# Optimization experiments

Measured on AMD Instinct MI355X. Metric: run time of the kernel, lower is better.

## Reference

```python
import jax, jax.numpy as jnp
import numpy as np
import math

DIM = 1024
N_HEADS = 16
HEAD_DIM = DIM // N_HEADS
FFN_HIDDEN = 4096
EPS = 1e-6


def setup_inputs() -> dict:
    key = jax.random.key(0)
    ks = jax.random.split(key, 10)
    s = 1.0 / math.sqrt(DIM)
    sh = 1.0 / math.sqrt(FFN_HIDDEN)
    return {
        "x": jax.random.normal(ks[0], (2, 2048, DIM), dtype=jnp.float32),
        # attention weights stored as [in, out] (y = x @ W)
        "wq": jax.random.normal(ks[1], (DIM, DIM), dtype=jnp.float32) * s,
        "wk": jax.random.normal(ks[2], (DIM, DIM), dtype=jnp.float32) * s,
        "wv": jax.random.normal(ks[3], (DIM, DIM), dtype=jnp.float32) * s,
        "wo": jax.random.normal(ks[4], (DIM, DIM), dtype=jnp.float32) * s,
        "w_gate": jax.random.normal(ks[5], (DIM, FFN_HIDDEN), dtype=jnp.float32) * s,
        "w_up": jax.random.normal(ks[6], (DIM, FFN_HIDDEN), dtype=jnp.float32) * s,
        "w_down": jax.random.normal(ks[7], (FFN_HIDDEN, DIM), dtype=jnp.float32) * sh,
        "attn_norm_w": jnp.ones((DIM,), dtype=jnp.float32),
        "ffn_norm_w": jnp.ones((DIM,), dtype=jnp.float32),
    }


def rmsnorm(x, w):
    xf = x.astype(jnp.float32)
    rms = jax.lax.rsqrt(jnp.mean(xf * xf, axis=-1, keepdims=True) + EPS)
    return (xf * rms).astype(x.dtype) * w


def attention(x, wq, wk, wv, wo):
    B, T, C = x.shape
    q = (x @ wq).reshape(B, T, N_HEADS, HEAD_DIM)
    k = (x @ wk).reshape(B, T, N_HEADS, HEAD_DIM)
    v = (x @ wv).reshape(B, T, N_HEADS, HEAD_DIM)
    scores = jnp.einsum("bqhd,bkhd->bhqk", q, k) / math.sqrt(HEAD_DIM)
    causal = jnp.tril(jnp.ones((T, T), dtype=bool))  # True = keep
    scores = jnp.where(causal, scores, -jnp.inf)
    attn = jax.nn.softmax(scores, axis=-1)
    out = jnp.einsum("bhqk,bkhd->bqhd", attn, v).reshape(B, T, C)
    return out @ wo


def swiglu(x, w_gate, w_up, w_down):
    return (jax.nn.silu(x @ w_gate) * (x @ w_up)) @ w_down


def reference(x, wq, wk, wv, wo, w_gate, w_up, w_down, attn_norm_w, ffn_norm_w):
    x = x + attention(rmsnorm(x, attn_norm_w), wq, wk, wv, wo)
    x = x + swiglu(rmsnorm(x, ffn_norm_w), w_gate, w_up, w_down)
    return x
```

## Files before the change

### kernel.cpp

```cpp
#include <hip/hip_runtime.h>
#include <hip/hip_bf16.h>
#include <stdint.h>
#include <math.h>

#define DIM   1024
#define TSEQ  2048
#define BATCH 2
#define NH    16
#define HD    64
#define FFN   4096
#define ROWS  (BATCH*TSEQ)
#define QKVN  (3*DIM)

typedef __attribute__((ext_vector_type(8))) short s16x8;
typedef __attribute__((ext_vector_type(4))) float f32x4;

__device__ __forceinline__ unsigned short f2bf(float f) {
  union { float f; unsigned u; } v; v.f = f;
  unsigned r = v.u + 0x7fffu + ((v.u >> 16) & 1u);
  return (unsigned short)(r >> 16);
}
__device__ __forceinline__ float bf2f(unsigned short h) {
  union { unsigned u; float f; } v; v.u = ((unsigned)h) << 16; return v.f;
}
__device__ __forceinline__ unsigned pack_bf2(float lo, float hi) {
  union { float f; unsigned u; } a, c; a.f = lo; c.f = hi;
  return (c.u & 0xffff0000u) | (a.u >> 16);
}

__device__ __forceinline__ void gld16(const void* g, void* l) {
  __builtin_amdgcn_global_load_lds((const __attribute__((address_space(1))) void*)g,
                                   (__attribute__((address_space(3))) void*)l, 16, 0, 0);
}

__device__ __forceinline__ int xcd_swz_flat() {
  const int nx = gridDim.x, ny = gridDim.y;
  const int nwg = nx * ny * gridDim.z;
  const int flat = blockIdx.x + nx * (blockIdx.y + ny * blockIdx.z);
  return (flat & 7) * (nwg >> 3) + (flat >> 3);
}

__global__ void wtrans_k(const float* __restrict__ w, unsigned short* __restrict__ wt,
                         int K, int N, int mode)
{
  __shared__ unsigned short t[64][65];
  const int n0 = blockIdx.x * 64, k0 = blockIdx.y * 64;
  const int tid = threadIdx.x;
  #pragma unroll
  for (int i = 0; i < 16; ++i) {
    const int r = i*4 + (tid >> 6), c = tid & 63;
    t[r][c] = f2bf(w[(size_t)(k0 + r) * N + n0 + c]);
  }
  __syncthreads();
  #pragma unroll
  for (int i = 0; i < 16; ++i) {
    const int r = i*4 + (tid >> 6), c = tid & 63;
    const int n = n0 + r;
    int dr = n;
    if (mode == 1) dr = ((n >> 4) << 5) + (n & 15);
    if (mode == 2) dr = ((n >> 4) << 5) + 16 + (n & 15);
    wt[(size_t)dr * K + k0 + c] = t[c][r];
  }
}

__global__ void wtrans_qkv_k(const float* __restrict__ wq, const float* __restrict__ wk,
                             const float* __restrict__ wv, unsigned short* __restrict__ wt)
{
  __shared__ unsigned short t[64][65];
  const int n0 = blockIdx.x * 64, k0 = blockIdx.y * 64, z = blockIdx.z;
  const float* w = (z == 0) ? wq : (z == 1) ? wk : wv;
  unsigned short* dst = wt + (size_t)z * DIM * DIM;
  const int tid = threadIdx.x;
  #pragma unroll
  for (int i = 0; i < 16; ++i) {
    const int r = i*4 + (tid >> 6), c = tid & 63;
    t[r][c] = f2bf(w[(size_t)(k0 + r) * DIM + n0 + c]);
  }
  __syncthreads();
  #pragma unroll
  for (int i = 0; i < 16; ++i) {
    const int r = i*4 + (tid >> 6), c = tid & 63;
    dst[(size_t)(n0 + r) * DIM + k0 + c] = t[c][r];
  }
}

__global__ void vtrans_k(const unsigned short* __restrict__ qkv, unsigned short* __restrict__ vt)
{
  __shared__ unsigned short t[64][65];
  const int tt0 = blockIdx.x * 64;
  const int bh = blockIdx.y, b = bh >> 4, h = bh & 15;
  const int tid = threadIdx.x;
  const unsigned short* src = qkv + (size_t)(b*TSEQ + tt0) * QKVN + 2*DIM + h*HD;
  #pragma unroll
  for (int i = 0; i < 16; ++i) {
    const int r = i*4 + (tid >> 6), c = tid & 63;
    t[r][c] = src[(size_t)r * QKVN + c];
  }
  __syncthreads();
  unsigned short* dst = vt + (size_t)bh * HD * TSEQ + tt0;
  #pragma unroll
  for (int i = 0; i < 16; ++i) {
    const int d = i*4 + (tid >> 6), c = tid & 63;
    dst[(size_t)d * TSEQ + c] = t[c][d];
  }
}

__global__ void rmsnorm_k(const float* __restrict__ x, const float* __restrict__ w,
                          unsigned short* __restrict__ o)
{
  const int row = blockIdx.x, tid = threadIdx.x;
  const float4 v = ((const float4*)(x + (size_t)row * DIM))[tid];
  float ss = v.x*v.x + v.y*v.y + v.z*v.z + v.w*v.w;
  #pragma unroll
  for (int off = 32; off >= 1; off >>= 1) ss += __shfl_xor(ss, off);
  __shared__ float sred[4];
  if ((tid & 63) == 0) sred[tid >> 6] = ss;
  __syncthreads();
  const float tot = sred[0] + sred[1] + sred[2] + sred[3];
  const float r = rsqrtf(tot * (1.0f/DIM) + 1e-6f);
  const float4 wv = ((const float4*)w)[tid];
  ushort4 ov;
  ov.x = f2bf(v.x*r*wv.x); ov.y = f2bf(v.y*r*wv.y);
  ov.z = f2bf(v.z*r*wv.z); ov.w = f2bf(v.w*r*wv.w);
  ((ushort4*)(o + (size_t)row * DIM))[tid] = ov;
}

__global__ void rmsnorm3_k(const float* __restrict__ x, const unsigned short* __restrict__ p0,
                           const unsigned short* __restrict__ p1, const float* __restrict__ w,
                           float* __restrict__ x1, unsigned short* __restrict__ o)
{
  const int row = blockIdx.x, tid = threadIdx.x;
  const size_t base = (size_t)row * DIM;
  const float4 a = ((const float4*)(x + base))[tid];
  const ushort4 b = ((const ushort4*)(p0 + base))[tid];
  const ushort4 c = ((const ushort4*)(p1 + base))[tid];
  float4 v;
  v.x = a.x + bf2f(b.x) + bf2f(c.x); v.y = a.y + bf2f(b.y) + bf2f(c.y);
  v.z = a.z + bf2f(b.z) + bf2f(c.z); v.w = a.w + bf2f(b.w) + bf2f(c.w);
  ((float4*)(x1 + base))[tid] = v;
  float ss = v.x*v.x + v.y*v.y + v.z*v.z + v.w*v.w;
  #pragma unroll
  for (int off = 32; off >= 1; off >>= 1) ss += __shfl_xor(ss, off);
  __shared__ float sred[4];
  if ((tid & 63) == 0) sred[tid >> 6] = ss;
  __syncthreads();
  const float tot = sred[0] + sred[1] + sred[2] + sred[3];
  const float r = rsqrtf(tot * (1.0f/DIM) + 1e-6f);
  const float4 wv = ((const float4*)w)[tid];
  ushort4 ov;
  ov.x = f2bf(v.x*r*wv.x); ov.y = f2bf(v.y*r*wv.y);
  ov.z = f2bf(v.z*r*wv.z); ov.w = f2bf(v.w*r*wv.w);
  ((ushort4*)(o + base))[tid] = ov;
}

__global__ void resadd5_k(const float* __restrict__ x1,
                          const unsigned short* __restrict__ q0, const unsigned short* __restrict__ q1,
                          const unsigned short* __restrict__ q2, const unsigned short* __restrict__ q3,
                          float* __restrict__ o)
{
  const size_t i = (size_t)blockIdx.x * 256 + threadIdx.x;
  const float4 a = ((const float4*)x1)[i];
  const ushort4 b = ((const ushort4*)q0)[i];
  const ushort4 c = ((const ushort4*)q1)[i];
  const ushort4 d = ((const ushort4*)q2)[i];
  const ushort4 e = ((const ushort4*)q3)[i];
  float4 v;
  v.x = a.x + bf2f(b.x) + bf2f(c.x) + bf2f(d.x) + bf2f(e.x);
  v.y = a.y + bf2f(b.y) + bf2f(c.y) + bf2f(d.y) + bf2f(e.y);
  v.z = a.z + bf2f(b.z) + bf2f(c.z) + bf2f(d.z) + bf2f(e.z);
  v.w = a.w + bf2f(b.w) + bf2f(c.w) + bf2f(d.w) + bf2f(e.w);
  ((float4*)o)[i] = v;
}

template<int NS>
__global__ void gemm128sp(const unsigned short* __restrict__ A, int lda,
                          const unsigned short* __restrict__ BT, int ldb,
                          unsigned short* __restrict__ P, int ldc, int Ksp)
{
  __shared__ __align__(16) unsigned short lA[128*64];
  __shared__ __align__(16) unsigned short lB[128*64];
  const int nx = gridDim.x, ny = gridDim.y;
  const int w = xcd_swz_flat();
  const int bx = w % nx, by = (w / nx) % ny, bz = w / (nx * ny);
  const int tid = threadIdx.x;
  const int lane = tid & 63;
  const int wid = tid >> 6;
  const int m0 = by * 128, n0 = bx * 128;
  const int Koff = bz * Ksp;
  P += (size_t)bz * ((size_t)ny * 128) * ldc;
  const int wr = (wid >> 1) * 64, wc = (wid & 1) * 64;
  const int lrow = lane & 15, lk8 = (lane >> 4) * 8;

  f32x4 acc[4][4] = {};

  for (int k0 = Koff; k0 < Koff + Ksp; k0 += 64) {
    #pragma unroll
    for (int c = 0; c < 4; ++c) {
      const int boff = c*4096 + tid*16;
      const int row = boff >> 7, colb = boff & 127;
      gld16((const char*)A + ((size_t)(m0+row)*lda + k0)*2 + colb, (char*)lA + boff);
    }
    #pragma unroll
    for (int c = 0; c < 4; ++c) {
      const int boff = c*4096 + tid*16;
      const int row = boff >> 7, colb = boff & 127;
      gld16((const char*)BT + ((size_t)(n0+row)*ldb + k0)*2 + colb, (char*)lB + boff);
    }
    __syncthreads();
    #pragma unroll
    for (int kk = 0; kk < 64; kk += 32) {
      s16x8 af[4], bf[4];
      #pragma unroll
      for (int i = 0; i < 4; ++i) af[i] = *(const s16x8*)&lA[(wr + i*16 + lrow)*64 + kk + lk8];
      #pragma unroll
      for (int j = 0; j < 4; ++j) bf[j] = *(const s16x8*)&lB[(wc + j*16 + lrow)*64 + kk + lk8];
      #pragma unroll
      for (int i = 0; i < 4; ++i)
        #pragma unroll
        for (int j = 0; j < 4; ++j)
          acc[i][j] = __builtin_amdgcn_mfma_f32_16x16x32_bf16(af[i], bf[j], acc[i][j], 0, 0, 0);
    }
    __syncthreads();
  }
  const int er = (lane >> 4) * 4, ec = lane & 15;
  #pragma unroll
  for (int i = 0; i < 4; ++i)
    #pragma unroll
    for (int j = 0; j < 4; ++j) {
      const int gr = m0 + wr + i*16 + er;
      const int gc = n0 + wc + j*16 + ec;
      #pragma unroll
      for (int e = 0; e < 4; ++e)
        P[(size_t)(gr + e) * ldc + gc] = f2bf(acc[i][j][e]);
    }
}

template<int EPI>
__global__ __launch_bounds__(512, 4) void gemm256(const unsigned short* __restrict__ A, int lda,
                                                  const unsigned short* __restrict__ BT, int ldb,
                                                  void* __restrict__ Cout, int ldc, int K,
                                                  int CX, int CY)
{
  __shared__ __align__(16) unsigned short lA[2][256*32];
  __shared__ __align__(16) unsigned short lB[2][128*32];
  const int nx = gridDim.x, ny = gridDim.y;
  const int flat = blockIdx.x + nx * blockIdx.y;
  const int xcd = flat & 7, kk_ = flat >> 3;
  const int RX = nx / CX, RY = ny / CY;
  const int cx = xcd % CX, cy = xcd / CX;
  const int bx = cx * RX + kk_ % RX;
  const int by = cy * RY + kk_ / RX;
  const int tid = threadIdx.x, lane = tid & 63, wid = tid >> 6;
  const int lrow = lane & 15, g = lane >> 4;
  const int wm = wid >> 1, wn = wid & 1;
  const int m0 = by * 256, n0 = bx * 128;

  const int pa = tid * 16;
  const int La = pa ^ (((pa >> 7) & 7) << 4);
  const int ra = La >> 6, kba = La & 63;
  const int Lb = La;
  const int rb = Lb >> 6, kbb = Lb & 63;
  const char* pA1 = (const char*)A + ((size_t)(m0 + ra) * lda) * 2 + kba;
  const char* pA2 = (const char*)A + ((size_t)(m0 + ra + 128) * lda) * 2 + kba;
  const char* pB1 = (const char*)BT + ((size_t)(n0 + rb) * ldb) * 2 + kbb;

#define STAGE(t) do { \
    char* dA_ = (char*)&lA[(t) & 1][0] + pa; \
    char* dB_ = (char*)&lB[(t) & 1][0] + pa; \
    const size_t kof_ = (size_t)(t) * 64; \
    gld16(pA1 + kof_, dA_); \
    gld16(pA2 + kof_, dA_ + 8192); \
    gld16(pB1 + kof_, dB_); \
  } while (0)

  const int aoff = (lrow * 64 + g * 16) ^ (((lrow >> 1) & 7) << 4);

  f32x4 acc[4][4] = {};
  s16x8 af[4], bf[4];

#define LGKM0()  do { asm volatile("s_waitcnt lgkmcnt(0)" ::: "memory"); \
                      __builtin_amdgcn_sched_barrier(0); } while (0)
#define VMCNT0() asm volatile("s_waitcnt vmcnt(0)" ::: "memory")
#define BARRIER() do { __builtin_amdgcn_s_barrier(); \
                       __builtin_amdgcn_sched_barrier(0); } while (0)

  const int NT = K >> 5;

  STAGE(0);
  VMCNT0();
  BARRIER();

  for (int t = 0; t < NT; ++t) {
    if (t + 1 < NT) STAGE(t + 1);
    const char* bufA = (const char*)&lA[t & 1][0] + wm * 4096;
    const char* bufB = (const char*)&lB[t & 1][0] + wn * 4096;
    #pragma unroll
    for (int i = 0; i < 4; ++i) af[i] = *(const s16x8*)(bufA + i*1024 + aoff);
    #pragma unroll
    for (int j = 0; j < 4; ++j) bf[j] = *(const s16x8*)(bufB + j*1024 + aoff);
    BARRIER();
    LGKM0();
    __builtin_amdgcn_s_setprio(1);
    #pragma unroll
    for (int i = 0; i < 4; ++i)
      #pragma unroll
      for (int j = 0; j < 4; ++j)
        acc[i][j] = __builtin_amdgcn_mfma_f32_16x16x32_bf16(af[i], bf[j], acc[i][j], 0, 0, 0);
    __builtin_amdgcn_s_setprio(0);
    VMCNT0();
    BARRIER();
  }

  const int er = g * 4, ec = lane & 15;
  if (EPI == 0) {
    unsigned short* C = (unsigned short*)Cout;
    #pragma unroll
    for (int i = 0; i < 4; ++i)
      #pragma unroll
      for (int j = 0; j < 4; ++j) {
        const int gr = m0 + wm*64 + i*16 + er;
        const int gc = n0 + wn*64 + j*16 + ec;
        #pragma unroll
        for (int e = 0; e < 4; ++e)
          C[(size_t)(gr + e) * ldc + gc] = f2bf(acc[i][j][e]);
      }
  } else {
    unsigned short* C = (unsigned short*)Cout;
    #pragma unroll
    for (int i = 0; i < 4; ++i)
      #pragma unroll
      for (int tp = 0; tp < 2; ++tp) {
        const int gr = m0 + wm*64 + i*16 + er;
        const int hc = (n0 >> 1) + wn*32 + tp*16 + ec;
        #pragma unroll
        for (int e = 0; e < 4; ++e) {
          const float gv = acc[i][2*tp][e];
          const float uv = acc[i][2*tp + 1][e];
          const float hv = gv / (1.f + __expf(-gv)) * uv;
          C[(size_t)(gr + e) * ldc + hc] = f2bf(hv);
        }
      }
  }
#undef STAGE
#undef LGKM0
#undef VMCNT0
#undef BARRIER
}

__global__ __launch_bounds__(512) void attn_fwd(const unsigned short* __restrict__ qkv,
                                                const unsigned short* __restrict__ vt,
                                                unsigned short* __restrict__ outp)
{
  __shared__ __align__(16) unsigned short lK[2][64*64];
  __shared__ __align__(16) unsigned short lV[2][64*64];
  const int nx = gridDim.x;
  const int wsz = xcd_swz_flat();
  const int qblk = wsz % nx;
  const int bh = wsz / nx, b = bh >> 4, h = bh & 15;
  const int tid = threadIdx.x, wid = tid >> 6, lane = tid & 63;
  const int lq = lane & 15, g = lane >> 4;

  const int qrow = qblk*128 + wid*16;
  const int myq = qrow + lq;

  const size_t qbase = ((size_t)(b*TSEQ + myq)) * QKVN + h*HD;
  const s16x8 qf0 = *(const s16x8*)&qkv[qbase + g*8];
  const s16x8 qf1 = *(const s16x8*)&qkv[qbase + 32 + g*8];

  const int boff = tid * 16;
  const int loff = boff ^ (((boff >> 7) & 7) << 4);
  const int srow = loff >> 7;
  const int scolb = loff & 127;
  const char* ksrc0 = (const char*)qkv +
      (((size_t)(b*TSEQ + srow)) * QKVN + DIM + h*HD) * 2 + scolb;
  const char* vsrc0 = (const char*)vt +
      (((size_t)bh*HD + srow) * TSEQ) * 2 + scolb;

  float mrun = -INFINITY, lrun = 0.f;
  f32x4 of[4] = {};

  const int nkt = 2*qblk + 2;

  gld16(ksrc0, (char*)lK[0] + boff);
  gld16(vsrc0, (char*)lV[0] + boff);
  int cur = 0;

  for (int kt = 0; kt < nkt; ++kt) {
    __syncthreads();
    if (kt + 1 < nkt) {
      gld16(ksrc0 + (size_t)(kt+1)*64*(QKVN*2), (char*)lK[cur^1] + boff);
      gld16(vsrc0 + (size_t)(kt+1)*128,         (char*)lV[cur^1] + boff);
    }
    if (kt*64 <= qrow + 15) {
      const unsigned short* Kb = lK[cur];
      const unsigned short* Vb = lV[cur];
      f32x4 sacc[4] = {};
      #pragma unroll
      for (int s = 0; s < 4; ++s) {
        const int r = s*16 + lq;
        const int sw = (r & 7) << 4;
        const s16x8 kf0 = *(const s16x8*)((const char*)Kb + r*128 + ((g*16) ^ sw));
        const s16x8 kf1 = *(const s16x8*)((const char*)Kb + r*128 + ((64 + g*16) ^ sw));
        sacc[s] = __builtin_amdgcn_mfma_f32_16x16x32_bf16(kf0, qf0, sacc[s], 0,0,0);
        sacc[s] = __builtin_amdgcn_mfma_f32_16x16x32_bf16(kf1, qf1, sacc[s], 0,0,0);
      }
      float p[4][4];
      float mt = -INFINITY;
      #pragma unroll
      for (int s = 0; s < 4; ++s)
        #pragma unroll
        for (int e = 0; e < 4; ++e) {
          const int key = kt*64 + s*16 + 4*g + e;
          const float v = (key <= myq) ? sacc[s][e]*0.125f : -INFINITY;
          p[s][e] = v;
          mt = fmaxf(mt, v);
        }
      mt = fmaxf(mt, __shfl_xor(mt, 16));
      mt = fmaxf(mt, __shfl_xor(mt, 32));
      const float mnew = fmaxf(mrun, mt);
      const float scale = __expf(mrun - mnew);
      float ssum = 0.f;
      #pragma unroll
      for (int s = 0; s < 4; ++s)
        #pragma unroll
        for (int e = 0; e < 4; ++e) {
          p[s][e] = __expf(p[s][e] - mnew);
          ssum += p[s][e];
        }
      ssum += __shfl_xor(ssum, 16);
      ssum += __shfl_xor(ssum, 32);
      lrun = lrun * scale + ssum;
      mrun = mnew;
      #pragma unroll
      for (int d0b = 0; d0b < 4; ++d0b) of[d0b] = of[d0b] * scale;
      #pragma unroll
      for (int hh = 0; hh < 2; ++hh) {
        unsigned w[4];
        #pragma unroll
        for (int j = 0; j < 4; ++j) w[j] = pack_bf2(p[2*hh][j], p[2*hh+1][j]);
        s16x8 bp;
        #pragma unroll
        for (int e = 0; e < 8; ++e) {
          const int srcg = 2*(g & 1) + (e >> 2);
          const unsigned ww = (unsigned)__shfl((int)w[e & 3], lq | (srcg << 4));
          bp[e] = (short)((g >= 2) ? (ww >> 16) : (ww & 0xffffu));
        }
        #pragma unroll
        for (int d0b = 0; d0b < 4; ++d0b) {
          const int r = d0b*16 + lq;
          const int sw = (r & 7) << 4;
          const s16x8 vf = *(const s16x8*)((const char*)Vb + r*128 + ((hh*64 + g*16) ^ sw));
          of[d0b] = __builtin_amdgcn_mfma_f32_16x16x32_bf16(vf, bp, of[d0b], 0,0,0);
        }
      }
    }
    cur ^= 1;
  }
  const float inv = 1.f / lrun;
  const size_t obase = ((size_t)(b*TSEQ + myq)) * DIM + h*HD;
  #pragma unroll
  for (int d0b = 0; d0b < 4; ++d0b) {
    ushort4 o;
    o.x = f2bf(of[d0b][0] * inv);
    o.y = f2bf(of[d0b][1] * inv);
    o.z = f2bf(of[d0b][2] * inv);
    o.w = f2bf(of[d0b][3] * inv);
    *(ushort4*)&outp[obase + d0b*16 + 4*g] = o;
  }
}

extern "C" void kernel_launch(void* const* d_in, const int* in_sizes, int n_in,
                              void* d_out, int out_size, void* d_ws, size_t ws_size,
                              hipStream_t stream)
{
  const float* x   = (const float*)d_in[0];
  const float* wq  = (const float*)d_in[1];
  const float* wk  = (const float*)d_in[2];
  const float* wv  = (const float*)d_in[3];
  const float* wo  = (const float*)d_in[4];
  const float* wg  = (const float*)d_in[5];
  const float* wu  = (const float*)d_in[6];
  const float* wd  = (const float*)d_in[7];
  const float* anw = (const float*)d_in[8];
  const float* fnw = (const float*)d_in[9];
  float* outp = (float*)d_out;

  const size_t MB = 1024*1024;
  const size_t RD = (size_t)ROWS * DIM;
  char* ws = (char*)d_ws;
  float*          x1    = (float*)         (ws + 0);
  unsigned short* wdT   = (unsigned short*)(ws + 16*MB);
  unsigned short* wguT  = (unsigned short*)(ws + 24*MB);
  unsigned short* wqkvT = (unsigned short*)(ws + 40*MB);
  unsigned short* woT   = (unsigned short*)(ws + 46*MB);
  unsigned short* xn    = (unsigned short*)(ws + 48*MB);
  unsigned short* qkv   = (unsigned short*)(ws + 56*MB);
  unsigned short* vtb   = (unsigned short*)(ws + 80*MB);
  unsigned short* aout  = (unsigned short*)(ws + 88*MB);
  unsigned short* pwo   = (unsigned short*)(ws + 56*MB);
  unsigned short* hbuf  = (unsigned short*)(ws + 56*MB);
  unsigned short* pdn   = (unsigned short*)(ws + 24*MB);

  const dim3 blk(256);

  wtrans_qkv_k<<<dim3(16,16,3), blk, 0, stream>>>(wq, wk, wv, wqkvT);
  wtrans_k<<<dim3(16,16), blk, 0, stream>>>(wo, woT, DIM, DIM, 0);
  wtrans_k<<<dim3(64,16), blk, 0, stream>>>(wg, wguT, DIM, FFN, 1);
  wtrans_k<<<dim3(64,16), blk, 0, stream>>>(wu, wguT, DIM, FFN, 2);
  wtrans_k<<<dim3(16,64), blk, 0, stream>>>(wd, wdT, FFN, DIM, 0);

  rmsnorm_k<<<ROWS, blk, 0, stream>>>(x, anw, xn);
  gemm256<0><<<dim3(QKVN/128, ROWS/256), dim3(512), 0, stream>>>(xn, DIM, wqkvT, DIM, qkv, QKVN, DIM, 4, 2);
  vtrans_k<<<dim3(TSEQ/64, BATCH*NH), blk, 0, stream>>>(qkv, vtb);
  attn_fwd<<<dim3(TSEQ/128, BATCH*NH), dim3(512), 0, stream>>>(qkv, vtb, aout);
  gemm128sp<2><<<dim3(DIM/128, ROWS/128, 2), blk, 0, stream>>>(aout, DIM, woT, DIM, pwo, DIM, DIM/2);
  rmsnorm3_k<<<ROWS, blk, 0, stream>>>(x, pwo, pwo + RD, fnw, x1, xn);

  gemm256<2><<<dim3(2*FFN/128, ROWS/256), dim3(512), 0, stream>>>(xn, DIM, wguT, DIM, hbuf, FFN, DIM, 4, 2);
  gemm128sp<4><<<dim3(DIM/128, ROWS/128, 4), blk, 0, stream>>>(hbuf, FFN, wdT, FFN, pdn, DIM, FFN/4);
  resadd5_k<<<dim3(ROWS*DIM/1024), blk, 0, stream>>>(x1, pdn, pdn + RD, pdn + 2*RD, pdn + 3*RD, outp);
}
```

Before: 306.5 us.

## Enlarge gemm256 tile to 256x256 with K=64 stages and interleaved load/MFMA schedule

The shared bf16 GEMM used for the QKV and gate/up projections now computes a 256x256 output tile per 512-thread block instead of 256x128. It stages 64-wide K slices. Each wave holds an 8x4 grid of 16x16 accumulators, and global-to-LDS loads are interleaved between MFMA quadrants behind barriers in an 8-wave ping-pong pattern. The aim is more arithmetic per byte loaded and better hiding of load latency. In exchange it uses about 128KB of LDS and more registers, which lowers occupancy, and it halves the block count, leaving the QKV GEMM with fewer blocks than CUs.

```diff
diff --git a/kernel.cpp b/kernel.cpp
--- a/kernel.cpp
+++ b/kernel.cpp
@@ -236,13 +236,13 @@
 }
 
 template<int EPI>
-__global__ __launch_bounds__(512, 4) void gemm256(const unsigned short* __restrict__ A, int lda,
+__global__ __launch_bounds__(512, 2) void gemm256(const unsigned short* __restrict__ A, int lda,
                                                   const unsigned short* __restrict__ BT, int ldb,
                                                   void* __restrict__ Cout, int ldc, int K,
                                                   int CX, int CY)
 {
-  __shared__ __align__(16) unsigned short lA[2][256*32];
-  __shared__ __align__(16) unsigned short lB[2][128*32];
+  __shared__ __align__(16) unsigned short lA[2][2][128*64];
+  __shared__ __align__(16) unsigned short lB[2][2][128*64];
   const int nx = gridDim.x, ny = gridDim.y;
   const int flat = blockIdx.x + nx * blockIdx.y;
   const int xcd = flat & 7, kk_ = flat >> 3;
@@ -252,73 +252,146 @@
   const int by = cy * RY + kk_ / RX;
   const int tid = threadIdx.x, lane = tid & 63, wid = tid >> 6;
   const int lrow = lane & 15, g = lane >> 4;
-  const int wm = wid >> 1, wn = wid & 1;
-  const int m0 = by * 256, n0 = bx * 128;
-
-  const int pa = tid * 16;
-  const int La = pa ^ (((pa >> 7) & 7) << 4);
-  const int ra = La >> 6, kba = La & 63;
-  const int Lb = La;
-  const int rb = Lb >> 6, kbb = Lb & 63;
-  const char* pA1 = (const char*)A + ((size_t)(m0 + ra) * lda) * 2 + kba;
-  const char* pA2 = (const char*)A + ((size_t)(m0 + ra + 128) * lda) * 2 + kba;
-  const char* pB1 = (const char*)BT + ((size_t)(n0 + rb) * ldb) * 2 + kbb;
-
-#define STAGE(t) do { \
-    char* dA_ = (char*)&lA[(t) & 1][0] + pa; \
-    char* dB_ = (char*)&lB[(t) & 1][0] + pa; \
-    const size_t kof_ = (size_t)(t) * 64; \
-    gld16(pA1 + kof_, dA_); \
-    gld16(pA2 + kof_, dA_ + 8192); \
-    gld16(pB1 + kof_, dB_); \
-  } while (0)
-
-  const int aoff = (lrow * 64 + g * 16) ^ (((lrow >> 1) & 7) << 4);
-
-  f32x4 acc[4][4] = {};
-  s16x8 af[4], bf[4];
-
+  const int wm = wid >> 2, wn = wid & 3;
+  const int m0 = by * 256, n0 = bx * 256;
+
+  const int p1 = tid * 16;
+  const int L1 = p1 ^ (((p1 >> 7) & 7) << 4);
+  const int r1 = L1 >> 7, c1 = L1 & 127;
+  const char* pAs = (const char*)A + ((size_t)(m0 + r1) * lda) * 2 + c1;
+  const char* pBs = (const char*)BT + ((size_t)(n0 + r1) * ldb) * 2 + c1;
+  const size_t a64 = (size_t)64 * lda * 2;
+  const size_t b64 = (size_t)64 * ldb * 2;
+
+#define STG_A(t, h) do { \
+    const char* s_ = pAs + (size_t)(h) * 2 * a64 + (size_t)(t) * 128; \
+    char* d_ = (char*)&lA[(t) & 1][h][0] + p1; \
+    gld16(s_, d_); gld16(s_ + a64, d_ + 8192); } while (0)
+#define STG_B(t, h) do { \
+    const char* s_ = pBs + (size_t)(h) * 2 * b64 + (size_t)(t) * 128; \
+    char* d_ = (char*)&lB[(t) & 1][h][0] + p1; \
+    gld16(s_, d_); gld16(s_ + b64, d_ + 8192); } while (0)
+
+  const int swz = (lrow & 7) << 4;
+  const int oK0 = (lrow * 128 + g * 16) ^ swz;
+  const int oK1 = (lrow * 128 + 64 + g * 16) ^ swz;
+  const char* bufA0 = (const char*)&lA[0][wm][0];
+  const char* bufA1 = (const char*)&lA[1][wm][0];
+  const char* bufB0 = (const char*)&lB[0][wn >> 1][0] + (wn & 1) * 8192;
+  const char* bufB1 = (const char*)&lB[1][wn >> 1][0] + (wn & 1) * 8192;
+
+  f32x4 acc[8][4] = {};
+  s16x8 a[8][2], b[4][2];
+
+#define RD_A_LO(B) do { _Pragma("unroll") for (int i_ = 0; i_ < 4; ++i_) { \
+    a[i_][0] = *(const s16x8*)((B) + i_*2048 + oK0); \
+    a[i_][1] = *(const s16x8*)((B) + i_*2048 + oK1); } } while (0)
+#define RD_A_HI(B) do { _Pragma("unroll") for (int i_ = 0; i_ < 4; ++i_) { \
+    a[4+i_][0] = *(const s16x8*)((B) + (4+i_)*2048 + oK0); \
+    a[4+i_][1] = *(const s16x8*)((B) + (4+i_)*2048 + oK1); } } while (0)
+#define RD_B01(B) do { _Pragma("unroll") for (int j_ = 0; j_ < 2; ++j_) { \
+    b[j_][0] = *(const s16x8*)((B) + j_*2048 + oK0); \
+    b[j_][1] = *(const s16x8*)((B) + j_*2048 + oK1); } } while (0)
+#define RD_B23(B) do { _Pragma("unroll") for (int j_ = 0; j_ < 2; ++j_) { \
+    b[2+j_][0] = *(const s16x8*)((B) + (2+j_)*2048 + oK0); \
+    b[2+j_][1] = *(const s16x8*)((B) + (2+j_)*2048 + oK1); } } while (0)
+
+#define MFMA_QD(IB, JB) do { \
+    __builtin_amdgcn_s_setprio(1); \
+    _Pragma("unroll") \
+    for (int i_ = 0; i_ < 4; ++i_) { \
+      _Pragma("unroll") \
+      for (int j_ = 0; j_ < 2; ++j_) { \
+        acc[(IB)+i_][(JB)+j_] = __builtin_amdgcn_mfma_f32_16x16x32_bf16(a[(IB)+i_][0], b[(JB)+j_][0], acc[(IB)+i_][(JB)+j_], 0,0,0); \
+        acc[(IB)+i_][(JB)+j_] = __builtin_amdgcn_mfma_f32_16x16x32_bf16(a[(IB)+i_][1], b[(JB)+j_][1], acc[(IB)+i_][(JB)+j_], 0,0,0); \
+      } } \
+    __builtin_amdgcn_s_setprio(0); } while (0)
+
+#define VMCNT(n) asm volatile("s_waitcnt vmcnt(" #n ")" ::: "memory")
 #define LGKM0()  do { asm volatile("s_waitcnt lgkmcnt(0)" ::: "memory"); \
                       __builtin_amdgcn_sched_barrier(0); } while (0)
-#define VMCNT0() asm volatile("s_waitcnt vmcnt(0)" ::: "memory")
 #define BARRIER() do { __builtin_amdgcn_s_barrier(); \
                        __builtin_amdgcn_sched_barrier(0); } while (0)
 
-  const int NT = K >> 5;
-
-  STAGE(0);
-  VMCNT0();
+  const int NT = K >> 6;
+  const int NI = NT >> 1;
+
+  STG_A(0, 0); STG_A(0, 1); STG_B(0, 0); STG_B(0, 1);
+  STG_A(1, 0); STG_A(1, 1);
+  VMCNT(4);
   BARRIER();
 
-  for (int t = 0; t < NT; ++t) {
-    if (t + 1 < NT) STAGE(t + 1);
-    const char* bufA = (const char*)&lA[t & 1][0] + wm * 4096;
-    const char* bufB = (const char*)&lB[t & 1][0] + wn * 4096;
-    #pragma unroll
-    for (int i = 0; i < 4; ++i) af[i] = *(const s16x8*)(bufA + i*1024 + aoff);
-    #pragma unroll
-    for (int j = 0; j < 4; ++j) bf[j] = *(const s16x8*)(bufB + j*1024 + aoff);
-    BARRIER();
+  for (int i = 0; i < NI - 1; ++i) {
+    const int u = 2 * i;
+    RD_A_LO(bufA0); RD_B01(bufB0);
+    STG_B(u + 1, 0);
+    BARRIER(); LGKM0();
+    MFMA_QD(0, 0);
+    BARRIER();
+    RD_A_HI(bufA0); RD_B23(bufB0);
+    STG_B(u + 1, 1);
+    BARRIER(); LGKM0();
+    MFMA_QD(0, 2);
+    BARRIER();
+    STG_A(u + 2, 0);
+    BARRIER();
+    MFMA_QD(4, 0);
+    BARRIER();
+    STG_A(u + 2, 1);
+    BARRIER();
+    MFMA_QD(4, 2);
+    VMCNT(4); BARRIER();
+    RD_A_LO(bufA1); RD_B01(bufB1);
+    STG_B(u + 2, 0);
+    BARRIER(); LGKM0();
+    MFMA_QD(0, 0);
+    BARRIER();
+    RD_A_HI(bufA1); RD_B23(bufB1);
+    STG_B(u + 2, 1);
+    BARRIER(); LGKM0();
+    MFMA_QD(0, 2);
+    BARRIER();
+    STG_A(u + 3, 0);
+    BARRIER();
+    MFMA_QD(4, 0);
+    BARRIER();
+    STG_A(u + 3, 1);
+    BARRIER();
+    MFMA_QD(4, 2);
+    VMCNT(4); BARRIER();
+  }
+  {
+    RD_A_LO(bufA0); RD_B01(bufB0);
+    STG_B(NT - 1, 0);
+    BARRIER(); LGKM0();
+    MFMA_QD(0, 0);
+    BARRIER();
+    RD_A_HI(bufA0); RD_B23(bufB0);
+    STG_B(NT - 1, 1);
+    BARRIER(); LGKM0();
+    MFMA_QD(0, 2);
+    BARRIER();
+    MFMA_QD(4, 0);
+    MFMA_QD(4, 2);
+    VMCNT(0); BARRIER();
+    RD_A_LO(bufA1); RD_B01(bufB1);
     LGKM0();
-    __builtin_amdgcn_s_setprio(1);
-    #pragma unroll
-    for (int i = 0; i < 4; ++i)
-      #pragma unroll
-      for (int j = 0; j < 4; ++j)
-        acc[i][j] = __builtin_amdgcn_mfma_f32_16x16x32_bf16(af[i], bf[j], acc[i][j], 0, 0, 0);
-    __builtin_amdgcn_s_setprio(0);
-    VMCNT0();
-    BARRIER();
+    MFMA_QD(0, 0);
+    RD_A_HI(bufA1); RD_B23(bufB1);
+    LGKM0();
+    MFMA_QD(0, 2);
+    MFMA_QD(4, 0);
+    MFMA_QD(4, 2);
   }
 
   const int er = g * 4, ec = lane & 15;
   if (EPI == 0) {
     unsigned short* C = (unsigned short*)Cout;
     #pragma unroll
-    for (int i = 0; i < 4; ++i)
+    for (int i = 0; i < 8; ++i)
       #pragma unroll
       for (int j = 0; j < 4; ++j) {
-        const int gr = m0 + wm*64 + i*16 + er;
+        const int gr = m0 + wm*128 + i*16 + er;
         const int gc = n0 + wn*64 + j*16 + ec;
         #pragma unroll
         for (int e = 0; e < 4; ++e)
@@ -327,10 +400,10 @@
   } else {
     unsigned short* C = (unsigned short*)Cout;
     #pragma unroll
-    for (int i = 0; i < 4; ++i)
+    for (int i = 0; i < 8; ++i)
       #pragma unroll
       for (int tp = 0; tp < 2; ++tp) {
-        const int gr = m0 + wm*64 + i*16 + er;
+        const int gr = m0 + wm*128 + i*16 + er;
         const int hc = (n0 >> 1) + wn*32 + tp*16 + ec;
         #pragma unroll
         for (int e = 0; e < 4; ++e) {
@@ -341,9 +414,15 @@
         }
       }
   }
-#undef STAGE
+#undef STG_A
+#undef STG_B
+#undef RD_A_LO
+#undef RD_A_HI
+#undef RD_B01
+#undef RD_B23
+#undef MFMA_QD
+#undef VMCNT
 #undef LGKM0
-#undef VMCNT0
 #undef BARRIER
 }
 
@@ -510,13 +589,13 @@
   wtrans_k<<<dim3(16,64), blk, 0, stream>>>(wd, wdT, FFN, DIM, 0);
 
   rmsnorm_k<<<ROWS, blk, 0, stream>>>(x, anw, xn);
-  gemm256<0><<<dim3(QKVN/128, ROWS/256), dim3(512), 0, stream>>>(xn, DIM, wqkvT, DIM, qkv, QKVN, DIM, 4, 2);
+  gemm256<0><<<dim3(QKVN/256, ROWS/256), dim3(512), 0, stream>>>(xn, DIM, wqkvT, DIM, qkv, QKVN, DIM, 4, 2);
   vtrans_k<<<dim3(TSEQ/64, BATCH*NH), blk, 0, stream>>>(qkv, vtb);
   attn_fwd<<<dim3(TSEQ/128, BATCH*NH), dim3(512), 0, stream>>>(qkv, vtb, aout);
   gemm128sp<2><<<dim3(DIM/128, ROWS/128, 2), blk, 0, stream>>>(aout, DIM, woT, DIM, pwo, DIM, DIM/2);
   rmsnorm3_k<<<ROWS, blk, 0, stream>>>(x, pwo, pwo + RD, fnw, x1, xn);
 
-  gemm256<2><<<dim3(2*FFN/128, ROWS/256), dim3(512), 0, stream>>>(xn, DIM, wguT, DIM, hbuf, FFN, DIM, 4, 2);
+  gemm256<2><<<dim3(2*FFN/256, ROWS/256), dim3(512), 0, stream>>>(xn, DIM, wguT, DIM, hbuf, FFN, DIM, 4, 2);
   gemm128sp<4><<<dim3(DIM/128, ROWS/128, 4), blk, 0, stream>>>(hbuf, FFN, wdT, FFN, pdn, DIM, FFN/4);
   resadd5_k<<<dim3(ROWS*DIM/1024), blk, 0, stream>>>(x1, pdn, pdn + RD, pdn + 2*RD, pdn + 3*RD, outp);
 }
```

Result: slower. 351.4 us (+14.6%).
